# Performance work log

Hardware: AMD Instinct MI355X
Metric: run time of the kernel (lower is better)

The kernel has to match this reference:

```python
import jax, jax.numpy as jnp
import numpy as np

B, H, W, C = 32, 56, 56, 192
WS, SH = 7, 3            # window size, shift size
NH = 6                   # num heads
HD = C // NH             # head dim = 32
N = WS * WS              # tokens per window = 49
NW = (H // WS) * (W // WS)  # windows per image = 64
HID = int(C * 4.0)       # MLP hidden = 768
EPS = 1e-6               # flax LayerNorm default


def _rel_index():
    # (N, N) int index into the (2*WS-1)^2 relative position bias table
    coords = np.stack(np.meshgrid(np.arange(WS), np.arange(WS), indexing='ij')).reshape(2, -1)
    rel = coords[:, :, None] - coords[:, None, :]          # (2, N, N)
    rel = rel.transpose(1, 2, 0) + (WS - 1)                # shift to >= 0
    idx = rel[..., 0] * (2 * WS - 1) + rel[..., 1]
    return jnp.asarray(idx, jnp.int32)


def _attn_mask():
    # standard Swin shifted-window mask: -100 between different regions
    img = np.zeros((H, W))
    cnt = 0
    for hs in (slice(0, -WS), slice(-WS, -SH), slice(-SH, None)):
        for ws in (slice(0, -WS), slice(-WS, -SH), slice(-SH, None)):
            img[hs, ws] = cnt
            cnt += 1
    win = img.reshape(H // WS, WS, W // WS, WS).transpose(0, 2, 1, 3).reshape(NW, N)
    diff = win[:, None, :] - win[:, :, None]
    return jnp.asarray(np.where(diff != 0, -100.0, 0.0), jnp.float32)


def setup_inputs() -> dict:
    key = jax.random.key(0)
    ks = jax.random.split(key, 8)
    s = 0.02
    return {
        'x': jax.random.normal(ks[0], (B, H, W, C), jnp.float32),
        'mask': _attn_mask(),
        'rel_index': _rel_index(),
        'ln1_scale': jnp.ones((C,), jnp.float32),
        'ln1_bias': jnp.zeros((C,), jnp.float32),
        'qkv_w': jax.random.normal(ks[1], (C, 3 * C), jnp.float32) * s,
        'qkv_b': jnp.zeros((3 * C,), jnp.float32),
        'rpb_table': jax.random.normal(ks[2], ((2 * WS - 1) ** 2, NH), jnp.float32) * s,
        'proj_w': jax.random.normal(ks[3], (C, C), jnp.float32) * s,
        'proj_b': jnp.zeros((C,), jnp.float32),
        'ln2_scale': jnp.ones((C,), jnp.float32),
        'ln2_bias': jnp.zeros((C,), jnp.float32),
        'mlp_w1': jax.random.normal(ks[4], (C, HID), jnp.float32) * s,
        'mlp_b1': jnp.zeros((HID,), jnp.float32),
        'mlp_w2': jax.random.normal(ks[5], (HID, C), jnp.float32) * s,
        'mlp_b2': jnp.zeros((C,), jnp.float32),
    }


def _ln(x, scale, bias):
    mu = jnp.mean(x, axis=-1, keepdims=True)
    var = jnp.mean(jnp.square(x - mu), axis=-1, keepdims=True)
    return (x - mu) * jax.lax.rsqrt(var + EPS) * scale + bias


def reference(x, mask, rel_index, ln1_scale, ln1_bias, qkv_w, qkv_b, rpb_table,
              proj_w, proj_b, ln2_scale, ln2_bias, mlp_w1, mlp_b1, mlp_w2, mlp_b2):
    # ---- W-MSA branch ----
    y = _ln(x, ln1_scale, ln1_bias)
    # cyclic shift (grid divisible by window -> pad_to_blocks is a no-op)
    y = jnp.roll(y, shift=(-SH, -SH), axis=(1, 2))
    # window partition: (B,H,W,C) -> (B*NW, N, C)
    y = y.reshape(B, H // WS, WS, W // WS, WS, C).transpose(0, 1, 3, 2, 4, 5)
    y = y.reshape(B * NW, N, C)
    # qkv: (B*NW, N, 3, NH, HD) -> q,k,v each (B*NW, NH, N, HD)
    qkv = (y @ qkv_w + qkv_b).reshape(B * NW, N, 3, NH, HD).transpose(2, 0, 3, 1, 4)
    q, k, v = qkv[0], qkv[1], qkv[2]
    attn = jnp.einsum('bhnd,bhmd->bhnm', q, k) * (HD ** -0.5)
    # relative position bias: (N,N,NH) -> (1,NH,N,N)
    attn = attn + rpb_table[rel_index].transpose(2, 0, 1)[None]
    # shifted-window mask: broadcast over batch and heads
    attn = attn.reshape(B, NW, NH, N, N) + mask[None, :, None]
    attn = jax.nn.softmax(attn.reshape(B * NW, NH, N, N), axis=-1)
    y = jnp.einsum('bhnm,bhmd->bhnd', attn, v).transpose(0, 2, 1, 3).reshape(B * NW, N, C)
    y = y @ proj_w + proj_b
    # window reverse and un-shift
    y = y.reshape(B, H // WS, W // WS, WS, WS, C).transpose(0, 1, 3, 2, 4, 5).reshape(B, H, W, C)
    y = jnp.roll(y, shift=(SH, SH), axis=(1, 2))
    x = x + y
    # ---- MLP branch ----
    z = _ln(x, ln2_scale, ln2_bias)
    z = jax.nn.gelu(z @ mlp_w1 + mlp_b1)  # flax nn.gelu default (tanh approx)
    z = z @ mlp_w2 + mlp_b2
    return x + z
```

## Files before the change

### kernel.cpp

```cpp
#include <hip/hip_runtime.h>


typedef __bf16 bf16_t;
typedef __bf16 bf16x8 __attribute__((ext_vector_type(8)));
typedef float  f32x4  __attribute__((ext_vector_type(4)));

__device__ inline float wred_sum(float v) {
#pragma unroll
  for (int o = 32; o; o >>= 1) v += __shfl_xor(v, o);
  return v;
}

__device__ inline float gelu_tanh(float x) {
  float u = 0.7978845608028654f * (x + 0.044715f * x * x * x);
  float e = __expf(2.f * u);
  float t = 1.f - 2.f / (e + 1.f);
  return 0.5f * x * (1.f + t);
}

__global__ __launch_bounds__(256) void k_ln1_win(
    const float* __restrict__ x, const float* __restrict__ sc,
    const float* __restrict__ bi, bf16_t* __restrict__ yw, int b0, int nTok) {
  int wv = (int)((blockIdx.x * 256 + threadIdx.x) >> 6);
  int lane = threadIdx.x & 63;
  if (wv >= nTok) return;
  int winL = wv / 49;
  int t = wv - winL * 49;
  int wi = winL & 63;
  int b = b0 + (winL >> 6);
  int t7 = t / 7;
  int hr = (wi >> 3) * 7 + t7;
  int wr = (wi & 7) * 7 + (t - t7 * 7);
  int h = hr + 3; if (h >= 56) h -= 56;
  int w = wr + 3; if (w >= 56) w -= 56;
  const float* xp = x + (((size_t)(b * 56 + h)) * 56 + w) * 192;
  float v0 = xp[lane], v1 = xp[lane + 64], v2 = xp[lane + 128];
  float s = wred_sum(v0 + v1 + v2);
  float q = wred_sum(v0 * v0 + v1 * v1 + v2 * v2);
  float mu = s * (1.f / 192.f);
  float var = q * (1.f / 192.f) - mu * mu;
  float rs = rsqrtf(var + 1e-6f);
  bf16_t* op = yw + (size_t)wv * 192;
  op[lane]       = (bf16_t)((v0 - mu) * rs * sc[lane]       + bi[lane]);
  op[lane + 64]  = (bf16_t)((v1 - mu) * rs * sc[lane + 64]  + bi[lane + 64]);
  op[lane + 128] = (bf16_t)((v2 - mu) * rs * sc[lane + 128] + bi[lane + 128]);
}

__global__ __launch_bounds__(256) void k_transpose_cvt(
    const float* __restrict__ in, bf16_t* __restrict__ out, int K, int N) {
  int idx = blockIdx.x * 256 + threadIdx.x;
  if (idx >= K * N) return;
  int n = idx / K, k = idx - n * K;
  out[idx] = (bf16_t)in[(size_t)k * N + n];
}

template <int K>
__global__ __launch_bounds__(256, 2) void k_gemm_bs(
    const bf16_t* __restrict__ A, const bf16_t* __restrict__ Bt,
    const float* __restrict__ bias, bf16_t* __restrict__ C, int Nn, int nMt) {
  constexpr int NKS = K / 32;
  int tid = threadIdx.x;
  int w = tid >> 6, lane = tid & 63;
  int c = lane & 15, g = lane >> 4;
  int bn = blockIdx.x;
  bf16x8 bf[4][NKS];
  const bf16_t* bp = Bt + (size_t)(bn * 64 + c) * K + 8 * g;
#pragma unroll
  for (int jc = 0; jc < 4; ++jc)
#pragma unroll
    for (int ks = 0; ks < NKS; ++ks)
      bf[jc][ks] = *(const bf16x8*)(bp + (size_t)jc * 16 * K + 32 * ks);
  float4 bias4[4];
#pragma unroll
  for (int jc = 0; jc < 4; ++jc)
    bias4[jc] = *(const float4*)(bias + bn * 64 + jc * 16 + 4 * g);
  for (int mt = blockIdx.y; mt < nMt; mt += gridDim.y) {
    int m0 = mt * 256 + w * 64;
    f32x4 acc[4][4] = {};
    const bf16_t* ap = A + (size_t)(m0 + c) * K + 8 * g;
#pragma unroll
    for (int ks = 0; ks < NKS; ++ks) {
      bf16x8 af[4];
#pragma unroll
      for (int ir = 0; ir < 4; ++ir)
        af[ir] = *(const bf16x8*)(ap + (size_t)ir * 16 * K + 32 * ks);
#pragma unroll
      for (int jc = 0; jc < 4; ++jc)
#pragma unroll
        for (int ir = 0; ir < 4; ++ir)
          acc[jc][ir] = __builtin_amdgcn_mfma_f32_16x16x32_bf16(
              bf[jc][ks], af[ir], acc[jc][ir], 0, 0, 0);
    }
#pragma unroll
    for (int ir = 0; ir < 4; ++ir) {
      bf16_t* cp = C + (size_t)(m0 + ir * 16 + c) * Nn + bn * 64 + 4 * g;
#pragma unroll
      for (int jc = 0; jc < 4; ++jc) {
        union { uint2 u; bf16_t e[4]; } pk;
#pragma unroll
        for (int r = 0; r < 4; ++r)
          pk.e[r] = (bf16_t)(acc[jc][ir][r] + ((const float*)&bias4[jc])[r]);
        *(uint2*)(cp + jc * 16) = pk.u;
      }
    }
  }
}

__global__ __launch_bounds__(64) void k_attn(
    const bf16_t* __restrict__ qkv, const int* __restrict__ relidx,
    const float* __restrict__ rpb, const float* __restrict__ mask,
    bf16_t* __restrict__ attn_out) {
  __shared__ char sm[8192];
  int blk = blockIdx.x;
  int wL = blk / 6, h = blk - wL * 6;
  int lane = threadIdx.x;
  int c = lane & 15, g = lane >> 4;
  {
    const float* mw = mask + (size_t)(wL & 63) * 2401;
    __bf16* bl = (__bf16*)sm;
    for (int idx = lane; idx < 2401; idx += 64)
      bl[idx] = (__bf16)(rpb[relidx[idx] * 6 + h] + mw[idx]);
  }
  const bf16_t* baseq = qkv + (size_t)wL * (49 * 576);
  f32x4 s[4][4] = {};
  bf16x8 qf[4], kf[4];
#pragma unroll
  for (int i = 0; i < 4; ++i) {
    int n = c + 16 * i; if (n > 48) n = 48;
    qf[i] = *(const bf16x8*)(baseq + (size_t)n * 576 + h * 32 + g * 8);
  }
#pragma unroll
  for (int j = 0; j < 4; ++j) {
    int m = c + 16 * j; if (m > 48) m = 48;
    kf[j] = *(const bf16x8*)(baseq + (size_t)m * 576 + 192 + h * 32 + g * 8);
  }
#pragma unroll
  for (int i = 0; i < 4; ++i)
#pragma unroll
    for (int j = 0; j < 4; ++j)
      s[i][j] = __builtin_amdgcn_mfma_f32_16x16x32_bf16(qf[i], kf[j], s[i][j],
                                                        0, 0, 0);
  const __bf16* bl = (const __bf16*)sm;
  float mxv[4][4], sum[4][4];
#pragma unroll
  for (int i = 0; i < 4; ++i)
#pragma unroll
    for (int r = 0; r < 4; ++r) {
      int n = 16 * i + 4 * g + r;
      int nc = n > 48 ? 48 : n;
      float best = -1e30f;
#pragma unroll
      for (int j = 0; j < 4; ++j) {
        int m = 16 * j + c;
        float v = -1e30f;
        if (m < 49)
          v = s[i][j][r] * 0.17677669529663687f + (float)bl[nc * 49 + m];
        s[i][j][r] = v;
        best = fmaxf(best, v);
      }
      mxv[i][r] = best;
    }
#pragma unroll
  for (int o = 8; o; o >>= 1)
#pragma unroll
    for (int i = 0; i < 4; ++i)
#pragma unroll
      for (int r = 0; r < 4; ++r)
        mxv[i][r] = fmaxf(mxv[i][r], __shfl_xor(mxv[i][r], o));
#pragma unroll
  for (int i = 0; i < 4; ++i)
#pragma unroll
    for (int r = 0; r < 4; ++r) {
      float ss = 0.f;
#pragma unroll
      for (int j = 0; j < 4; ++j) {
        float p = __expf(s[i][j][r] - mxv[i][r]);
        s[i][j][r] = p;
        ss += p;
      }
      sum[i][r] = ss;
    }
#pragma unroll
  for (int o = 8; o; o >>= 1)
#pragma unroll
    for (int i = 0; i < 4; ++i)
#pragma unroll
      for (int r = 0; r < 4; ++r)
        sum[i][r] += __shfl_xor(sum[i][r], o);
#pragma unroll
  for (int i = 0; i < 4; ++i)
#pragma unroll
    for (int j = 0; j < 4; ++j)
#pragma unroll
      for (int r = 0; r < 4; ++r) {
        int n = 16 * i + 4 * g + r;
        int m = 16 * j + c;
        int offb = n * 128 + ((2 * m) ^ ((n & 7) << 4));
        *(__bf16*)(sm + offb) = (__bf16)s[i][j][r];
      }
  f32x4 o2[4][2] = {};
#pragma unroll
  for (int kt = 0; kt < 2; ++kt) {
    bf16x8 pf[4], vf[2];
#pragma unroll
    for (int i = 0; i < 4; ++i) {
      int n = c + 16 * i;
      int cb = (16 * g + 64 * kt) ^ ((n & 7) << 4);
      pf[i] = *(const bf16x8*)(sm + n * 128 + cb);
    }
#pragma unroll
    for (int dt = 0; dt < 2; ++dt) {
      int d = c + 16 * dt;
      union { bf16x8 v; __bf16 e[8]; } u;
#pragma unroll
      for (int e0 = 0; e0 < 8; ++e0) {
        int m = 8 * g + e0 + 32 * kt; if (m > 48) m = 48;
        u.e[e0] = baseq[(size_t)m * 576 + 384 + h * 32 + d];
      }
      vf[dt] = u.v;
    }
#pragma unroll
    for (int i = 0; i < 4; ++i)
#pragma unroll
      for (int dt = 0; dt < 2; ++dt)
        o2[i][dt] = __builtin_amdgcn_mfma_f32_16x16x32_bf16(pf[i], vf[dt],
                                                            o2[i][dt], 0, 0, 0);
  }
#pragma unroll
  for (int i = 0; i < 4; ++i)
#pragma unroll
    for (int dt = 0; dt < 2; ++dt)
#pragma unroll
      for (int r = 0; r < 4; ++r) {
        int n = 16 * i + 4 * g + r;
        if (n < 49) {
          int d = 16 * dt + c;
          attn_out[((size_t)wL * 49 + n) * 192 + h * 32 + d] =
              (bf16_t)(o2[i][dt][r] / sum[i][r]);
        }
      }
}

__global__ __launch_bounds__(256) void k_unwin_ln2(
    const float* __restrict__ x, const bf16_t* __restrict__ projw,
    const float* __restrict__ sc, const float* __restrict__ bi,
    float* __restrict__ out, bf16_t* __restrict__ z, int b0, int nTok) {
  int wv = (int)((blockIdx.x * 256 + threadIdx.x) >> 6);
  int lane = threadIdx.x & 63;
  if (wv >= nTok) return;
  int bL = wv / 3136;
  int rem = wv - bL * 3136;
  int hh = rem / 56, ww2 = rem - hh * 56;
  int b = b0 + bL;
  int hr = hh + 53; if (hr >= 56) hr -= 56;
  int wr = ww2 + 53; if (wr >= 56) wr -= 56;
  int winL = bL * 64 + (hr / 7) * 8 + (wr / 7);
  int t = (hr % 7) * 7 + (wr % 7);
  const bf16_t* pp = projw + ((size_t)winL * 49 + t) * 192;
  size_t gtok = ((size_t)(b * 56 + hh)) * 56 + ww2;
  const float* xp = x + gtok * 192;
  float v0 = xp[lane]       + (float)pp[lane];
  float v1 = xp[lane + 64]  + (float)pp[lane + 64];
  float v2 = xp[lane + 128] + (float)pp[lane + 128];
  float* op = out + gtok * 192;
  op[lane] = v0; op[lane + 64] = v1; op[lane + 128] = v2;
  float s = wred_sum(v0 + v1 + v2);
  float q = wred_sum(v0 * v0 + v1 * v1 + v2 * v2);
  float mu = s * (1.f / 192.f);
  float var = q * (1.f / 192.f) - mu * mu;
  float rs = rsqrtf(var + 1e-6f);
  bf16_t* zp = z + gtok * 192;
  zp[lane]       = (bf16_t)((v0 - mu) * rs * sc[lane]       + bi[lane]);
  zp[lane + 64]  = (bf16_t)((v1 - mu) * rs * sc[lane + 64]  + bi[lane + 64]);
  zp[lane + 128] = (bf16_t)((v2 - mu) * rs * sc[lane + 128] + bi[lane + 128]);
}

__global__ __launch_bounds__(256, 2) void k_mlp_fused2(
    const bf16_t* __restrict__ z, const bf16_t* __restrict__ w1T,
    const float* __restrict__ b1, const bf16_t* __restrict__ w2T,
    const float* __restrict__ b2, float* __restrict__ out) {
  __shared__ char hsm[16384];
  int tid = threadIdx.x;
  int wv = tid >> 6, lane = tid & 63;
  int c = lane & 15, g = lane >> 4;
  char* wbase = hsm + wv * 4096;
  int row0 = blockIdx.x * 128 + wv * 32;

  bf16x8 zfr[2][6];
  const bf16_t* zp = z + (size_t)(row0 + c) * 192 + 8 * g;
#pragma unroll
  for (int ir = 0; ir < 2; ++ir)
#pragma unroll
    for (int ks = 0; ks < 6; ++ks)
      zfr[ir][ks] = *(const bf16x8*)(zp + (size_t)ir * 16 * 192 + 32 * ks);

  f32x4 acc2[12][2] = {};

  for (int hc = 0; hc < 12; ++hc) {
    f32x4 acc1[4][2] = {};
    const bf16_t* w1p = w1T + (size_t)(hc * 64 + c) * 192 + 8 * g;
#pragma unroll
    for (int ks = 0; ks < 6; ++ks) {
      bf16x8 wf[4];
#pragma unroll
      for (int jh = 0; jh < 4; ++jh)
        wf[jh] = *(const bf16x8*)(w1p + (size_t)jh * 16 * 192 + 32 * ks);
#pragma unroll
      for (int jh = 0; jh < 4; ++jh)
#pragma unroll
        for (int ir = 0; ir < 2; ++ir)
          acc1[jh][ir] = __builtin_amdgcn_mfma_f32_16x16x32_bf16(
              wf[jh], zfr[ir][ks], acc1[jh][ir], 0, 0, 0);
    }
#pragma unroll
    for (int jh = 0; jh < 4; ++jh) {
      float4 b1v = *(const float4*)(b1 + hc * 64 + jh * 16 + 4 * g);
#pragma unroll
      for (int ir = 0; ir < 2; ++ir) {
        union { uint2 u; __bf16 e[4]; } pk;
#pragma unroll
        for (int r = 0; r < 4; ++r)
          pk.e[r] = (__bf16)gelu_tanh(acc1[jh][ir][r] + ((const float*)&b1v)[r]);
        int rl = ir * 16 + c;
        *(uint2*)(wbase + rl * 128 + ((32 * jh + 8 * g) ^ ((rl & 7) << 4))) =
            pk.u;
      }
    }
    const bf16_t* w2p = w2T + (size_t)c * 768 + hc * 64 + 8 * g;
#pragma unroll
    for (int ks2 = 0; ks2 < 2; ++ks2) {
      bf16x8 af[2];
#pragma unroll
      for (int ir = 0; ir < 2; ++ir) {
        int rl = ir * 16 + c;
        af[ir] = *(const bf16x8*)(wbase + rl * 128 +
                                  ((64 * ks2 + 16 * g) ^ ((rl & 7) << 4)));
      }
      bf16x8 wf2[12];
#pragma unroll
      for (int jc = 0; jc < 12; ++jc)
        wf2[jc] = *(const bf16x8*)(w2p + (size_t)jc * 16 * 768 + 32 * ks2);
#pragma unroll
      for (int jc = 0; jc < 12; ++jc)
#pragma unroll
        for (int ir = 0; ir < 2; ++ir)
          acc2[jc][ir] = __builtin_amdgcn_mfma_f32_16x16x32_bf16(
              wf2[jc], af[ir], acc2[jc][ir], 0, 0, 0);
    }
  }
#pragma unroll
  for (int jc = 0; jc < 12; ++jc) {
    float4 b2v = *(const float4*)(b2 + jc * 16 + 4 * g);
#pragma unroll
    for (int ir = 0; ir < 2; ++ir) {
      int row = row0 + ir * 16 + c;
      float* op = out + (size_t)row * 192 + jc * 16 + 4 * g;
      float4 cur = *(float4*)op;
      cur.x += acc2[jc][ir][0] + b2v.x;
      cur.y += acc2[jc][ir][1] + b2v.y;
      cur.z += acc2[jc][ir][2] + b2v.z;
      cur.w += acc2[jc][ir][3] + b2v.w;
      *(float4*)op = cur;
    }
  }
}

extern "C" void kernel_launch(void* const* d_in, const int* in_sizes, int n_in,
                              void* d_out, int out_size, void* d_ws,
                              size_t ws_size, hipStream_t stream) {
  (void)in_sizes; (void)n_in; (void)out_size;
  const float* x     = (const float*)d_in[0];
  const float* maskp = (const float*)d_in[1];
  const int*   reli  = (const int*)d_in[2];
  const float* ln1s  = (const float*)d_in[3];
  const float* ln1b  = (const float*)d_in[4];
  const float* qkvw  = (const float*)d_in[5];
  const float* qkvb  = (const float*)d_in[6];
  const float* rpb   = (const float*)d_in[7];
  const float* projw = (const float*)d_in[8];
  const float* projb = (const float*)d_in[9];
  const float* ln2s  = (const float*)d_in[10];
  const float* ln2b  = (const float*)d_in[11];
  const float* w1    = (const float*)d_in[12];
  const float* b1    = (const float*)d_in[13];
  const float* w2    = (const float*)d_in[14];
  const float* b2    = (const float*)d_in[15];
  float* out = (float*)d_out;

  auto aup = [](size_t v) { return (v + 255) & ~(size_t)255; };
  char* base = (char*)d_ws;
  size_t off = 0;
  bf16_t* z_buf = (bf16_t*)(base + off); off += aup((size_t)100352 * 192 * 2);
  bf16_t* qkvT  = (bf16_t*)(base + off); off += aup((size_t)576 * 192 * 2);
  bf16_t* projT = (bf16_t*)(base + off); off += aup((size_t)192 * 192 * 2);
  bf16_t* w1T   = (bf16_t*)(base + off); off += aup((size_t)768 * 192 * 2);
  bf16_t* w2T   = (bf16_t*)(base + off); off += aup((size_t)192 * 768 * 2);
  size_t offB = off;

  int Bc = 32;
  while (Bc > 4 && offB + (size_t)Bc * 3136 * (576 + 192) * 2 > ws_size)
    Bc >>= 1;
  bf16_t* bufB = (bf16_t*)(base + offB);
  bf16_t* bufA = (bf16_t*)(base + offB + aup((size_t)Bc * 3136 * 576 * 2));

  k_transpose_cvt<<<(192 * 576 + 255) / 256, 256, 0, stream>>>(qkvw, qkvT, 192, 576);
  k_transpose_cvt<<<(192 * 192 + 255) / 256, 256, 0, stream>>>(projw, projT, 192, 192);
  k_transpose_cvt<<<(192 * 768 + 255) / 256, 256, 0, stream>>>(w1, w1T, 192, 768);
  k_transpose_cvt<<<(768 * 192 + 255) / 256, 256, 0, stream>>>(w2, w2T, 768, 192);

  for (int b0 = 0; b0 < 32; b0 += Bc) {
    int nTok = Bc * 3136, nWin = Bc * 64;
    int nMt = nTok / 256;
    k_ln1_win<<<nTok / 4, 256, 0, stream>>>(x, ln1s, ln1b, bufA, b0, nTok);
    {
      int nbn = 576 / 64;
      int gy = (512 + nbn - 1) / nbn; if (gy > nMt) gy = nMt;
      k_gemm_bs<192><<<dim3(nbn, gy), 256, 0, stream>>>(bufA, qkvT, qkvb, bufB,
                                                        576, nMt);
    }
    k_attn<<<nWin * 6, 64, 0, stream>>>(bufB, reli, rpb, maskp, bufA);
    {
      int nbn = 192 / 64;
      int gy = (512 + nbn - 1) / nbn; if (gy > nMt) gy = nMt;
      k_gemm_bs<192><<<dim3(nbn, gy), 256, 0, stream>>>(bufA, projT, projb,
                                                        bufB, 192, nMt);
    }
    k_unwin_ln2<<<nTok / 4, 256, 0, stream>>>(x, bufB, ln2s, ln2b, out, z_buf,
                                              b0, nTok);
  }

  k_mlp_fused2<<<100352 / 128, 256, 0, stream>>>(z_buf, w1T, b1, w2T, b2, out);
}
```

Measured before the change: 755.5 us.

## Precompute head-major rel-pos bias, stage V transposed in LDS, double-buffer MLP hidden tile

A small setup kernel gathers the relative position bias into a per-head contiguous table, so the attention kernel no longer does an indirect gather per element. The attention kernel now loads V with vector reads into a swizzled transposed LDS tile, replacing scalar strided global loads when building the PV operands. The fused MLP kernel double-buffers its hidden-activation LDS tile, doubling shared memory per block, and issues the W2 fragment loads earlier to overlap them with GELU and the LDS writes. These changes raise LDS use and register pressure, which could reduce occupancy.

```diff
diff --git a/kernel.cpp b/kernel.cpp
--- a/kernel.cpp
+++ b/kernel.cpp
@@ -54,6 +54,15 @@
   out[idx] = (bf16_t)in[(size_t)k * N + n];
 }
 
+__global__ __launch_bounds__(256) void k_rpb(
+    const int* __restrict__ relidx, const float* __restrict__ rpb,
+    float* __restrict__ rpbh) {
+  int idx = blockIdx.x * 256 + threadIdx.x;
+  if (idx >= 6 * 2401) return;
+  int h = idx / 2401, n = idx - h * 2401;
+  rpbh[idx] = rpb[relidx[n] * 6 + h];
+}
+
 template <int K>
 __global__ __launch_bounds__(256, 2) void k_gemm_bs(
     const bf16_t* __restrict__ A, const bf16_t* __restrict__ Bt,
@@ -107,21 +116,45 @@
 }
 
 __global__ __launch_bounds__(64) void k_attn(
-    const bf16_t* __restrict__ qkv, const int* __restrict__ relidx,
-    const float* __restrict__ rpb, const float* __restrict__ mask,
-    bf16_t* __restrict__ attn_out) {
-  __shared__ char sm[8192];
+    const bf16_t* __restrict__ qkv, const float* __restrict__ rpbh,
+    const float* __restrict__ mask, bf16_t* __restrict__ attn_out) {
+  __shared__ char sm[12288];
   int blk = blockIdx.x;
   int wL = blk / 6, h = blk - wL * 6;
   int lane = threadIdx.x;
   int c = lane & 15, g = lane >> 4;
+  const bf16_t* baseq = qkv + (size_t)wL * (49 * 576);
+
   {
     const float* mw = mask + (size_t)(wL & 63) * 2401;
+    const float* bh = rpbh + (size_t)h * 2401;
     __bf16* bl = (__bf16*)sm;
     for (int idx = lane; idx < 2401; idx += 64)
-      bl[idx] = (__bf16)(rpb[relidx[idx] * 6 + h] + mw[idx]);
-  }
-  const bf16_t* baseq = qkv + (size_t)wL * (49 * 576);
+      bl[idx] = (__bf16)(bh[idx] + mw[idx]);
+  }
+
+  char* vts = sm + 8192;
+  {
+    uint4 z4 = {0u, 0u, 0u, 0u};
+#pragma unroll
+    for (int it = 0; it < 4; ++it)
+      *(uint4*)(vts + lane * 16 + it * 1024) = z4;
+#pragma unroll
+    for (int it = 0; it < 4; ++it) {
+      int task = lane + 64 * it;
+      if (task < 196) {
+        int m = task % 49, dc = task / 49;
+        union { bf16x8 v; __bf16 e[8]; } u;
+        u.v = *(const bf16x8*)(baseq + (size_t)m * 576 + 384 + h * 32 + dc * 8);
+#pragma unroll
+        for (int e0 = 0; e0 < 8; ++e0) {
+          int d = dc * 8 + e0;
+          *(__bf16*)(vts + d * 128 + ((2 * m) ^ ((d & 7) << 4))) = u.e[e0];
+        }
+      }
+    }
+  }
+
   f32x4 s[4][4] = {};
   bf16x8 qf[4], kf[4];
 #pragma unroll
@@ -140,6 +173,7 @@
     for (int j = 0; j < 4; ++j)
       s[i][j] = __builtin_amdgcn_mfma_f32_16x16x32_bf16(qf[i], kf[j], s[i][j],
                                                         0, 0, 0);
+
   const __bf16* bl = (const __bf16*)sm;
   float mxv[4][4], sum[4][4];
 #pragma unroll
@@ -187,6 +221,7 @@
 #pragma unroll
       for (int r = 0; r < 4; ++r)
         sum[i][r] += __shfl_xor(sum[i][r], o);
+
 #pragma unroll
   for (int i = 0; i < 4; ++i)
 #pragma unroll
@@ -198,6 +233,7 @@
         int offb = n * 128 + ((2 * m) ^ ((n & 7) << 4));
         *(__bf16*)(sm + offb) = (__bf16)s[i][j][r];
       }
+
   f32x4 o2[4][2] = {};
 #pragma unroll
   for (int kt = 0; kt < 2; ++kt) {
@@ -211,13 +247,8 @@
 #pragma unroll
     for (int dt = 0; dt < 2; ++dt) {
       int d = c + 16 * dt;
-      union { bf16x8 v; __bf16 e[8]; } u;
-#pragma unroll
-      for (int e0 = 0; e0 < 8; ++e0) {
-        int m = 8 * g + e0 + 32 * kt; if (m > 48) m = 48;
-        u.e[e0] = baseq[(size_t)m * 576 + 384 + h * 32 + d];
-      }
-      vf[dt] = u.v;
+      vf[dt] = *(const bf16x8*)(vts + d * 128 +
+                                ((64 * kt + 16 * g) ^ ((d & 7) << 4)));
     }
 #pragma unroll
     for (int i = 0; i < 4; ++i)
@@ -226,6 +257,7 @@
         o2[i][dt] = __builtin_amdgcn_mfma_f32_16x16x32_bf16(pf[i], vf[dt],
                                                             o2[i][dt], 0, 0, 0);
   }
+
 #pragma unroll
   for (int i = 0; i < 4; ++i)
 #pragma unroll
@@ -275,15 +307,15 @@
   zp[lane + 128] = (bf16_t)((v2 - mu) * rs * sc[lane + 128] + bi[lane + 128]);
 }
 
-__global__ __launch_bounds__(256, 2) void k_mlp_fused2(
+__global__ __launch_bounds__(256, 2) void k_mlp_fused3(
     const bf16_t* __restrict__ z, const bf16_t* __restrict__ w1T,
     const float* __restrict__ b1, const bf16_t* __restrict__ w2T,
     const float* __restrict__ b2, float* __restrict__ out) {
-  __shared__ char hsm[16384];
+  __shared__ char hsm[32768];
   int tid = threadIdx.x;
   int wv = tid >> 6, lane = tid & 63;
   int c = lane & 15, g = lane >> 4;
-  char* wbase = hsm + wv * 4096;
+  char* wbase = hsm + wv * 8192;
   int row0 = blockIdx.x * 128 + wv * 32;
 
   bf16x8 zfr[2][6];
@@ -296,7 +328,9 @@
 
   f32x4 acc2[12][2] = {};
 
+#pragma unroll 2
   for (int hc = 0; hc < 12; ++hc) {
+    char* hbuf = wbase + (hc & 1) * 4096;
     f32x4 acc1[4][2] = {};
     const bf16_t* w1p = w1T + (size_t)(hc * 64 + c) * 192 + 8 * g;
 #pragma unroll
@@ -312,6 +346,11 @@
           acc1[jh][ir] = __builtin_amdgcn_mfma_f32_16x16x32_bf16(
               wf[jh], zfr[ir][ks], acc1[jh][ir], 0, 0, 0);
     }
+    const bf16_t* w2p = w2T + (size_t)c * 768 + hc * 64 + 8 * g;
+    bf16x8 wf2a[12];
+#pragma unroll
+    for (int jc = 0; jc < 12; ++jc)
+      wf2a[jc] = *(const bf16x8*)(w2p + (size_t)jc * 16 * 768);
 #pragma unroll
     for (int jh = 0; jh < 4; ++jh) {
       float4 b1v = *(const float4*)(b1 + hc * 64 + jh * 16 + 4 * g);
@@ -322,30 +361,43 @@
         for (int r = 0; r < 4; ++r)
           pk.e[r] = (__bf16)gelu_tanh(acc1[jh][ir][r] + ((const float*)&b1v)[r]);
         int rl = ir * 16 + c;
-        *(uint2*)(wbase + rl * 128 + ((32 * jh + 8 * g) ^ ((rl & 7) << 4))) =
+        *(uint2*)(hbuf + rl * 128 + ((32 * jh + 8 * g) ^ ((rl & 7) << 4))) =
             pk.u;
       }
     }
-    const bf16_t* w2p = w2T + (size_t)c * 768 + hc * 64 + 8 * g;
-#pragma unroll
-    for (int ks2 = 0; ks2 < 2; ++ks2) {
+    {
       bf16x8 af[2];
 #pragma unroll
       for (int ir = 0; ir < 2; ++ir) {
         int rl = ir * 16 + c;
-        af[ir] = *(const bf16x8*)(wbase + rl * 128 +
-                                  ((64 * ks2 + 16 * g) ^ ((rl & 7) << 4)));
-      }
-      bf16x8 wf2[12];
-#pragma unroll
-      for (int jc = 0; jc < 12; ++jc)
-        wf2[jc] = *(const bf16x8*)(w2p + (size_t)jc * 16 * 768 + 32 * ks2);
+        af[ir] = *(const bf16x8*)(hbuf + rl * 128 +
+                                  ((16 * g) ^ ((rl & 7) << 4)));
+      }
 #pragma unroll
       for (int jc = 0; jc < 12; ++jc)
 #pragma unroll
         for (int ir = 0; ir < 2; ++ir)
           acc2[jc][ir] = __builtin_amdgcn_mfma_f32_16x16x32_bf16(
-              wf2[jc], af[ir], acc2[jc][ir], 0, 0, 0);
+              wf2a[jc], af[ir], acc2[jc][ir], 0, 0, 0);
+    }
+    {
+      bf16x8 wf2b[12];
+#pragma unroll
+      for (int jc = 0; jc < 12; ++jc)
+        wf2b[jc] = *(const bf16x8*)(w2p + (size_t)jc * 16 * 768 + 32);
+      bf16x8 af[2];
+#pragma unroll
+      for (int ir = 0; ir < 2; ++ir) {
+        int rl = ir * 16 + c;
+        af[ir] = *(const bf16x8*)(hbuf + rl * 128 +
+                                  ((64 + 16 * g) ^ ((rl & 7) << 4)));
+      }
+#pragma unroll
+      for (int jc = 0; jc < 12; ++jc)
+#pragma unroll
+        for (int ir = 0; ir < 2; ++ir)
+          acc2[jc][ir] = __builtin_amdgcn_mfma_f32_16x16x32_bf16(
+              wf2b[jc], af[ir], acc2[jc][ir], 0, 0, 0);
     }
   }
 #pragma unroll
@@ -395,6 +447,7 @@
   bf16_t* projT = (bf16_t*)(base + off); off += aup((size_t)192 * 192 * 2);
   bf16_t* w1T   = (bf16_t*)(base + off); off += aup((size_t)768 * 192 * 2);
   bf16_t* w2T   = (bf16_t*)(base + off); off += aup((size_t)192 * 768 * 2);
+  float*  rpbh  = (float*)(base + off);  off += aup((size_t)6 * 2401 * 4);
   size_t offB = off;
 
   int Bc = 32;
@@ -407,6 +460,7 @@
   k_transpose_cvt<<<(192 * 192 + 255) / 256, 256, 0, stream>>>(projw, projT, 192, 192);
   k_transpose_cvt<<<(192 * 768 + 255) / 256, 256, 0, stream>>>(w1, w1T, 192, 768);
   k_transpose_cvt<<<(768 * 192 + 255) / 256, 256, 0, stream>>>(w2, w2T, 768, 192);
+  k_rpb<<<(6 * 2401 + 255) / 256, 256, 0, stream>>>(reli, rpb, rpbh);
 
   for (int b0 = 0; b0 < 32; b0 += Bc) {
     int nTok = Bc * 3136, nWin = Bc * 64;
@@ -418,7 +472,7 @@
       k_gemm_bs<192><<<dim3(nbn, gy), 256, 0, stream>>>(bufA, qkvT, qkvb, bufB,
                                                         576, nMt);
     }
-    k_attn<<<nWin * 6, 64, 0, stream>>>(bufB, reli, rpb, maskp, bufA);
+    k_attn<<<nWin * 6, 64, 0, stream>>>(bufB, rpbh, maskp, bufA);
     {
       int nbn = 192 / 64;
       int gy = (512 + nbn - 1) / nbn; if (gy > nMt) gy = nMt;
@@ -429,5 +483,5 @@
                                               b0, nTok);
   }
 
-  k_mlp_fused2<<<100352 / 128, 256, 0, stream>>>(z_buf, w1T, b1, w2T, b2, out);
-}
+  k_mlp_fused3<<<100352 / 128, 256, 0, stream>>>(z_buf, w1T, b1, w2T, b2, out);
+}
```

Result: slower. 787.7 us (+4.3%).
